# Performance work log

Hardware: AMD Instinct MI355X
Metric: run time of the kernel (lower is better)

## Reference

```python
import jax, jax.numpy as jnp
import numpy as np

B, D0, D1 = 4096, 128, 128
T, DEPTH, W = 64, 2, 4          # num_tree, depth, width
S = W ** (DEPTH + 1)            # num_state = 64
NODES = sum(W ** l for l in range(DEPTH + 1))  # 21 internal nodes per tree
D = D0 + D1


def setup_inputs() -> dict:
    key = jax.random.key(0)
    ks = jax.random.split(key, 9)
    inp0 = jax.random.normal(ks[0], (B, D0), jnp.float32)
    inp1 = jax.random.normal(ks[1], (B, D1), jnp.float32)
    x2 = jax.random.normal(ks[2], (B,), jnp.float32)
    # ForestLinear: per-tree, per-node linear maps to `width` branch logits
    W_nodes = 0.02 * jax.random.normal(ks[3], (T, NODES, D, W), jnp.float32)
    b_nodes = jnp.zeros((T, NODES, W), jnp.float32)
    # MultiDense([0,1], 1): per-(tree,state) linear probe per input
    W0 = 0.02 * jax.random.normal(ks[4], (T, S, D0), jnp.float32)
    b0 = jnp.zeros((T, S), jnp.float32)
    W1 = 0.02 * jax.random.normal(ks[5], (T, S, D1), jnp.float32)
    b1 = jnp.zeros((T, S), jnp.float32)
    return {"inp0": inp0, "inp1": inp1, "x2": x2,
            "W_nodes": W_nodes, "b_nodes": b_nodes,
            "W0": W0, "b0": b0, "W1": W1, "b1": b1}


def _forest_states(x, W_nodes, b_nodes):
    # x: [B, D] -> leaf-state probabilities [B, T, S]
    logits = jnp.einsum('bd,tndw->btnw', x, W_nodes) + b_nodes  # [B,T,NODES,W]
    probs = jax.nn.softmax(logits, axis=-1)
    p = jnp.ones((x.shape[0], T, 1), probs.dtype)
    off = 0
    for l in range(DEPTH + 1):
        n = W ** l
        pl = probs[:, :, off:off + n, :]                 # [B,T,n,W]
        p = (p[..., None] * pl).reshape(x.shape[0], T, n * W)
        off += n
    return p  # [B, T, S]


def reference(inp0, inp1, x2, W_nodes, b_nodes, W0, b0, W1, b1):
    x_states = _forest_states(jnp.concatenate([inp0, inp1], axis=-1), W_nodes, b_nodes)
    # per-tree/state linear probes; equivalent to tile + MultiDense, no materialized tile
    x_pred = (jnp.einsum('bd,tsd->bts', inp0, W0) + b0
              + jnp.einsum('bd,tsd->bts', inp1, W1) + b1)  # [B,T,S]
    y_pred_logit_parallel = x2[:, None, None] + x_pred
    ave_pred_tree = jnp.sum(x_states * jax.nn.sigmoid(y_pred_logit_parallel), axis=2)  # [B,T]
    ave_pred = jnp.mean(ave_pred_tree, axis=1)  # [B]
    return (y_pred_logit_parallel, ave_pred)
```

## Files before the change

kernel.cpp:

```cpp
#include <hip/hip_runtime.h>

#define B_SZ    4096
#define DD      256
#define T_TREES 64
#define NNODES  21
#define S_LEAF  64
#define NCOL_L  84
#define PRED_OFF 96
#define NCOL    160
#define M_TILE  128
#define HBYTES  (NCOL * 128 * 2)
#define WBYTES  (2 * HBYTES)
#define XOFF    ((size_t)T_TREES * WBYTES)
#define PRSTR   150

typedef __attribute__((ext_vector_type(8))) short  short8;
typedef __attribute__((ext_vector_type(4))) float  f32x4;

__device__ __forceinline__ unsigned short f2bf(float f) {
    unsigned int u = __float_as_uint(f);
    u += 0x7fffu + ((u >> 16) & 1u);
    return (unsigned short)(u >> 16);
}
__device__ __forceinline__ float bf2f(unsigned short u) {
    return __uint_as_float((unsigned int)u << 16);
}
__device__ __forceinline__ void gl2lds16(const void* g, void* l) {
    __builtin_amdgcn_global_load_lds(
        (const __attribute__((address_space(1))) unsigned int*)g,
        (__attribute__((address_space(3))) unsigned int*)l, 16, 0, 0);
}
__device__ __forceinline__ int woff(int c, int klo) {
    return c * 256 + ((klo ^ (c & 15)) << 4);
}

__global__ void zero_ave_kernel(float* __restrict__ out1) {
    int i = blockIdx.x * 256 + threadIdx.x;
    if (i < B_SZ) out1[i] = 0.0f;
}

__global__ void prep_weights(const float* __restrict__ Wn, const float* __restrict__ W0,
                             const float* __restrict__ W1, const float* __restrict__ inp0,
                             const float* __restrict__ inp1, char* __restrict__ ws,
                             float* __restrict__ out1) {
    int id = blockIdx.x * 256 + threadIdx.x;
    if (id < 43008) {
        int oct  = id & 31;
        int rest = id >> 5;
        int n    = rest % NNODES;
        int t    = rest / NNODES;
        int h    = oct >> 4, klo = oct & 15;
        const f32x4* src = (const f32x4*)(Wn + (((size_t)t * NNODES + n) * DD + oct * 8) * 4);
        f32x4 v[8];
        #pragma unroll
        for (int j = 0; j < 8; ++j) v[j] = src[j];
        char* base = ws + (size_t)t * WBYTES + h * HBYTES;
        #pragma unroll
        for (int w = 0; w < 4; ++w) {
            int c = n * 4 + w;
            short8 pack;
            #pragma unroll
            for (int j = 0; j < 8; ++j) pack[j] = (short)f2bf(v[j][w]);
            *(short8*)(base + woff(c, klo)) = pack;
        }
    } else if (id < 67584) {
        int idx  = id - 43008;
        int klo  = idx & 15;
        int h    = (idx >> 4) & 1;
        int rest = idx >> 5;
        int c    = NCOL_L + rest % 12;
        int t    = rest / 12;
        short8 z = (short8){0,0,0,0,0,0,0,0};
        *(short8*)(ws + (size_t)t * WBYTES + h * HBYTES + woff(c, klo)) = z;
    } else if (id < 198656) {
        int idx = id - 67584;
        int klo = idx & 15;
        int h   = (idx >> 4) & 1;
        int s   = (idx >> 5) & 63;
        int t   = idx >> 11;
        const float* src = (h == 0) ? (W0 + ((size_t)t * S_LEAF + s) * 128 + klo * 8)
                                    : (W1 + ((size_t)t * S_LEAF + s) * 128 + klo * 8);
        short8 pack;
        #pragma unroll
        for (int j = 0; j < 8; ++j) pack[j] = (short)f2bf(src[j]);
        *(short8*)(ws + (size_t)t * WBYTES + h * HBYTES + woff(PRED_OFF + s, klo)) = pack;
    } else if (id < 202752) {
        out1[id - 198656] = 0.0f;
    } else if (id < 333824) {
        int idx = id - 202752;
        int oct = idx & 31;
        int r   = idx >> 5;
        const float* src = (oct < 16) ? (inp0 + (size_t)r * 128 + oct * 8)
                                      : (inp1 + (size_t)r * 128 + (oct - 16) * 8);
        f32x4 f0 = *(const f32x4*)src;
        f32x4 f1 = *(const f32x4*)(src + 4);
        short8 pack;
        pack[0]=(short)f2bf(f0[0]); pack[1]=(short)f2bf(f0[1]);
        pack[2]=(short)f2bf(f0[2]); pack[3]=(short)f2bf(f0[3]);
        pack[4]=(short)f2bf(f1[0]); pack[5]=(short)f2bf(f1[1]);
        pack[6]=(short)f2bf(f1[2]); pack[7]=(short)f2bf(f1[3]);
        *(short8*)(ws + XOFF + ((size_t)r * DD + oct * 8) * 2) = pack;
    }
}

template<bool PRE>
__device__ __forceinline__ short8 ldA(const unsigned short* __restrict__ xbf,
                                      const float* __restrict__ inp0,
                                      const float* __restrict__ inp1,
                                      int gr, int kk, int kg) {
    if (PRE) {
        return *(const short8*)(xbf + (size_t)gr * DD + kk * 32 + kg * 8);
    } else {
        int k0 = kk * 32 + kg * 8;
        const float* src = (kk < 4) ? (inp0 + (size_t)gr * 128 + k0)
                                    : (inp1 + (size_t)gr * 128 + (k0 - 128));
        f32x4 f0 = *(const f32x4*)src;
        f32x4 f1 = *(const f32x4*)(src + 4);
        short8 a;
        a[0]=(short)f2bf(f0[0]); a[1]=(short)f2bf(f0[1]);
        a[2]=(short)f2bf(f0[2]); a[3]=(short)f2bf(f0[3]);
        a[4]=(short)f2bf(f1[0]); a[5]=(short)f2bf(f1[1]);
        a[6]=(short)f2bf(f1[2]); a[7]=(short)f2bf(f1[3]);
        return a;
    }
}

template<bool PRE>
__global__ __launch_bounds__(256, 4)
void forest_main(const float* __restrict__ inp0, const float* __restrict__ inp1,
                 const float* __restrict__ x2,   const float* __restrict__ Wn,
                 const float* __restrict__ bn,   const float* __restrict__ W0,
                 const float* __restrict__ b0,   const float* __restrict__ W1,
                 const float* __restrict__ b1,   const char* __restrict__ wsW,
                 float* __restrict__ out0, float* __restrict__ out1) {
    __shared__ __align__(16) char smem[HBYTES];

    const int tid  = threadIdx.x;
    const int orig = blockIdx.x;
    const int swz  = (orig & 7) * 256 + (orig >> 3);
    const int t    = swz >> 5;
    const int mt   = swz & 31;
    const int m0   = mt * M_TILE;
    const int lane = tid & 63;
    const int wid  = tid >> 6;
    const int ri   = lane & 15;
    const int kg   = lane >> 4;

    const unsigned short* xbf = (const unsigned short*)(wsW + XOFF);

    f32x4 acc[2][10];
    #pragma unroll
    for (int sr = 0; sr < 2; ++sr)
        #pragma unroll
        for (int ct = 0; ct < 10; ++ct)
            acc[sr][ct] = (f32x4){0.f, 0.f, 0.f, 0.f};

    const int baseRow = m0 + wid * 32;
    const int grA = baseRow + ri;
    const int grB = baseRow + 16 + ri;

    short8 aC0 = ldA<PRE>(xbf, inp0, inp1, grA, 0, kg);
    short8 aC1 = ldA<PRE>(xbf, inp0, inp1, grB, 0, kg);

    for (int h = 0; h < 2; ++h) {
        if (PRE) {
            const char* src = wsW + (size_t)t * WBYTES + h * HBYTES + tid * 16;
            char* dst = smem + tid * 16;
            #pragma unroll
            for (int it = 0; it < 10; ++it)
                gl2lds16(src + it * 4096, dst + it * 4096);
        } else {
            #pragma unroll
            for (int it = 0; it < 10; ++it) {
                int q   = tid + it * 256;
                int c   = q >> 4;
                int klo = q & 15;
                int k0  = h * 128 + klo * 8;
                unsigned short v[8];
                if (c < NCOL_L) {
                    int n = c >> 2, w = c & 3;
                    const float* src = Wn + (((size_t)t * NNODES + n) * DD + k0) * 4 + w;
                    #pragma unroll
                    for (int j = 0; j < 8; ++j) v[j] = f2bf(src[j * 4]);
                } else if (c < PRED_OFF) {
                    #pragma unroll
                    for (int j = 0; j < 8; ++j) v[j] = 0;
                } else {
                    int s = c - PRED_OFF;
                    const float* src = (k0 < 128) ? (W0 + ((size_t)t * S_LEAF + s) * 128 + k0)
                                                  : (W1 + ((size_t)t * S_LEAF + s) * 128 + (k0 - 128));
                    #pragma unroll
                    for (int j = 0; j < 8; ++j) v[j] = f2bf(src[j]);
                }
                short8 pack;
                #pragma unroll
                for (int j = 0; j < 8; ++j) pack[j] = (short)v[j];
                *(short8*)(smem + woff(c, klo)) = pack;
            }
        }
        __syncthreads();

        #pragma unroll
        for (int ks = 0; ks < 4; ++ks) {
            const int kk = h * 4 + ks;
            short8 aN0, aN1;
            if (kk < 7) {
                aN0 = ldA<PRE>(xbf, inp0, inp1, grA, kk + 1, kg);
                aN1 = ldA<PRE>(xbf, inp0, inp1, grB, kk + 1, kg);
            }
            #pragma unroll
            for (int ct = 0; ct < 10; ++ct) {
                short8 b = *(const short8*)(smem + woff(ct * 16 + ri, ks * 4 + kg));
                acc[0][ct] = __builtin_amdgcn_mfma_f32_16x16x32_bf16(aC0, b, acc[0][ct], 0, 0, 0);
                acc[1][ct] = __builtin_amdgcn_mfma_f32_16x16x32_bf16(aC1, b, acc[1][ct], 0, 0, 0);
            }
            aC0 = aN0; aC1 = aN1;
        }
        __syncthreads();
    }

    unsigned short* pr = (unsigned short*)smem;

    #pragma unroll
    for (int sr = 0; sr < 2; ++sr) {
        const int rlBase = wid * 32 + sr * 16 + kg * 4;
        #pragma unroll
        for (int ct = 0; ct < 6; ++ct) {
            int c = ct * 16 + ri;
            bool valid = (c < NCOL_L);
            float bnv = valid ? bn[t * NCOL_L + c] : 0.0f;
            #pragma unroll
            for (int r = 0; r < 4; ++r) {
                float v = acc[sr][ct][r] + bnv;
                float e = __expf(v);
                float ss = e + __shfl_xor(e, 1);
                ss += __shfl_xor(ss, 2);
                float p = e * __builtin_amdgcn_rcpf(ss);
                if (valid) pr[(rlBase + r) * PRSTR + c] = f2bf(p);
            }
        }
        const int gr0 = m0 + rlBase;
        float x2v0 = x2[gr0], x2v1 = x2[gr0 + 1], x2v2 = x2[gr0 + 2], x2v3 = x2[gr0 + 3];
        #pragma unroll
        for (int ct = 0; ct < 4; ++ct) {
            int s = ct * 16 + ri;
            float bb = b0[t * S_LEAF + s] + b1[t * S_LEAF + s];
            #pragma unroll
            for (int r = 0; r < 4; ++r) {
                float xv = (r == 0) ? x2v0 : (r == 1) ? x2v1 : (r == 2) ? x2v2 : x2v3;
                float y = acc[sr][ct + 6][r] + xv + bb;
                out0[((size_t)(gr0 + r) * T_TREES + t) * S_LEAF + s] = y;
                float sg = __builtin_amdgcn_rcpf(1.0f + __expf(-y));
                pr[(rlBase + r) * PRSTR + NCOL_L + s] = f2bf(sg);
            }
        }
    }
    __syncthreads();

    {
        int rl = wid * 32 + (lane >> 1);
        int hh = lane & 1;
        const unsigned short* prow = pr + (size_t)rl * PRSTR;
        float ssum = 0.0f;
        #pragma unroll
        for (int b8 = 0; b8 < 8; ++b8) {
            int b = hh * 8 + b8;
            float p01 = bf2f(prow[b >> 2]) * bf2f(prow[4 + b]);
            float inner = 0.0f;
            #pragma unroll
            for (int j = 0; j < 4; ++j) {
                int s = 4 * b + j;
                inner += bf2f(prow[20 + s]) * bf2f(prow[NCOL_L + s]);
            }
            ssum += p01 * inner;
        }
        ssum += __shfl_xor(ssum, 1);
        if (hh == 0) atomicAdd(out1 + (m0 + rl), ssum * (1.0f / T_TREES));
    }
}

extern "C" void kernel_launch(void* const* d_in, const int* in_sizes, int n_in,
                              void* d_out, int out_size, void* d_ws, size_t ws_size,
                              hipStream_t stream) {
    const float* inp0 = (const float*)d_in[0];
    const float* inp1 = (const float*)d_in[1];
    const float* x2   = (const float*)d_in[2];
    const float* Wn   = (const float*)d_in[3];
    const float* bn   = (const float*)d_in[4];
    const float* W0   = (const float*)d_in[5];
    const float* b0   = (const float*)d_in[6];
    const float* W1   = (const float*)d_in[7];
    const float* b1   = (const float*)d_in[8];

    float* out0 = (float*)d_out;
    float* out1 = out0 + (size_t)B_SZ * T_TREES * S_LEAF;

    const size_t need = XOFF + (size_t)B_SZ * DD * 2;
    dim3 grid((B_SZ / M_TILE) * T_TREES);

    if (ws_size >= need) {
        hipLaunchKernelGGL(prep_weights, dim3(1305), dim3(256), 0, stream,
                           Wn, W0, W1, inp0, inp1, (char*)d_ws, out1);
        hipLaunchKernelGGL((forest_main<true>), grid, dim3(256), 0, stream,
                           inp0, inp1, x2, Wn, bn, W0, b0, W1, b1,
                           (const char*)d_ws, out0, out1);
    } else {
        hipLaunchKernelGGL(zero_ave_kernel, dim3((B_SZ + 255) / 256), dim3(256), 0, stream, out1);
        hipLaunchKernelGGL((forest_main<false>), grid, dim3(256), 0, stream,
                           inp0, inp1, x2, Wn, bn, W0, b0, W1, b1,
                           (const char*)nullptr, out0, out1);
    }
}
```

Baseline: 55.74 us.

## Double-buffer K-quarter weight tiles and compute tree epilogue in registers via shuffles

Splits the per-tree weight slab into four K-quarters and double-buffers them in LDS, so the next quarter's global-to-LDS load overlaps the MFMAs of the current one. The column layout is reordered so level-0/1 nodes sit in the first tiles, with a new pair-interleaved swizzle. The epilogue no longer writes probabilities to LDS and rereads them after a barrier. It builds leaf path probabilities with cross-lane shuffles and reduces them into partial sums before the atomics. The cost is more barriers, more shuffle traffic and more register pressure.

```diff
diff --git a/kernel.cpp b/kernel.cpp
--- a/kernel.cpp
+++ b/kernel.cpp
@@ -5,14 +5,12 @@
 #define T_TREES 64
 #define NNODES  21
 #define S_LEAF  64
-#define NCOL_L  84
-#define PRED_OFF 96
 #define NCOL    160
 #define M_TILE  128
-#define HBYTES  (NCOL * 128 * 2)
-#define WBYTES  (2 * HBYTES)
+#define QBYTES  20480
+#define WBYTES  (4 * QBYTES)
 #define XOFF    ((size_t)T_TREES * WBYTES)
-#define PRSTR   150
+
 
 typedef __attribute__((ext_vector_type(8))) short  short8;
 typedef __attribute__((ext_vector_type(4))) float  f32x4;
@@ -22,16 +20,13 @@
     u += 0x7fffu + ((u >> 16) & 1u);
     return (unsigned short)(u >> 16);
 }
-__device__ __forceinline__ float bf2f(unsigned short u) {
-    return __uint_as_float((unsigned int)u << 16);
-}
 __device__ __forceinline__ void gl2lds16(const void* g, void* l) {
     __builtin_amdgcn_global_load_lds(
         (const __attribute__((address_space(1))) unsigned int*)g,
         (__attribute__((address_space(3))) unsigned int*)l, 16, 0, 0);
 }
-__device__ __forceinline__ int woff(int c, int klo) {
-    return c * 256 + ((klo ^ (c & 15)) << 4);
+__device__ __host__ __forceinline__ int woffq(int c, int klo) {
+    return (c >> 1) * 256 + (((((klo << 1) ^ (c & 14))) | (c & 1)) << 4);
 }
 
 __global__ void zero_ave_kernel(float* __restrict__ out1) {
@@ -49,41 +44,40 @@
         int rest = id >> 5;
         int n    = rest % NNODES;
         int t    = rest / NNODES;
-        int h    = oct >> 4, klo = oct & 15;
+        int q    = oct >> 3, klo = oct & 7;
         const f32x4* src = (const f32x4*)(Wn + (((size_t)t * NNODES + n) * DD + oct * 8) * 4);
         f32x4 v[8];
         #pragma unroll
         for (int j = 0; j < 8; ++j) v[j] = src[j];
-        char* base = ws + (size_t)t * WBYTES + h * HBYTES;
+        char* base = ws + (size_t)t * WBYTES + q * QBYTES;
         #pragma unroll
         for (int w = 0; w < 4; ++w) {
-            int c = n * 4 + w;
+            int c = n * 4 + w + (n >= 5 ? 12 : 0);
             short8 pack;
             #pragma unroll
             for (int j = 0; j < 8; ++j) pack[j] = (short)f2bf(v[j][w]);
-            *(short8*)(base + woff(c, klo)) = pack;
+            *(short8*)(base + woffq(c, klo)) = pack;
         }
     } else if (id < 67584) {
         int idx  = id - 43008;
-        int klo  = idx & 15;
-        int h    = (idx >> 4) & 1;
+        int kc   = idx & 31;
         int rest = idx >> 5;
-        int c    = NCOL_L + rest % 12;
+        int c    = 20 + rest % 12;
         int t    = rest / 12;
         short8 z = (short8){0,0,0,0,0,0,0,0};
-        *(short8*)(ws + (size_t)t * WBYTES + h * HBYTES + woff(c, klo)) = z;
+        *(short8*)(ws + (size_t)t * WBYTES + (kc >> 3) * QBYTES + woffq(c, kc & 7)) = z;
     } else if (id < 198656) {
         int idx = id - 67584;
-        int klo = idx & 15;
-        int h   = (idx >> 4) & 1;
+        int kc  = idx & 31;
         int s   = (idx >> 5) & 63;
         int t   = idx >> 11;
-        const float* src = (h == 0) ? (W0 + ((size_t)t * S_LEAF + s) * 128 + klo * 8)
-                                    : (W1 + ((size_t)t * S_LEAF + s) * 128 + klo * 8);
+        int k0  = kc * 8;
+        const float* src = (k0 < 128) ? (W0 + ((size_t)t * S_LEAF + s) * 128 + k0)
+                                      : (W1 + ((size_t)t * S_LEAF + s) * 128 + (k0 - 128));
         short8 pack;
         #pragma unroll
         for (int j = 0; j < 8; ++j) pack[j] = (short)f2bf(src[j]);
-        *(short8*)(ws + (size_t)t * WBYTES + h * HBYTES + woff(PRED_OFF + s, klo)) = pack;
+        *(short8*)(ws + (size_t)t * WBYTES + (kc >> 3) * QBYTES + woffq(96 + s, kc & 7)) = pack;
     } else if (id < 202752) {
         out1[id - 198656] = 0.0f;
     } else if (id < 333824) {
@@ -103,26 +97,20 @@
     }
 }
 
-template<bool PRE>
-__device__ __forceinline__ short8 ldA(const unsigned short* __restrict__ xbf,
-                                      const float* __restrict__ inp0,
-                                      const float* __restrict__ inp1,
-                                      int gr, int kk, int kg) {
-    if (PRE) {
-        return *(const short8*)(xbf + (size_t)gr * DD + kk * 32 + kg * 8);
-    } else {
-        int k0 = kk * 32 + kg * 8;
-        const float* src = (kk < 4) ? (inp0 + (size_t)gr * 128 + k0)
-                                    : (inp1 + (size_t)gr * 128 + (k0 - 128));
-        f32x4 f0 = *(const f32x4*)src;
-        f32x4 f1 = *(const f32x4*)(src + 4);
-        short8 a;
-        a[0]=(short)f2bf(f0[0]); a[1]=(short)f2bf(f0[1]);
-        a[2]=(short)f2bf(f0[2]); a[3]=(short)f2bf(f0[3]);
-        a[4]=(short)f2bf(f1[0]); a[5]=(short)f2bf(f1[1]);
-        a[6]=(short)f2bf(f1[2]); a[7]=(short)f2bf(f1[3]);
-        return a;
-    }
+__device__ __forceinline__ short8 ldAraw(const float* __restrict__ inp0,
+                                         const float* __restrict__ inp1,
+                                         int gr, int kkidx, int kg) {
+    int k0 = kkidx * 32 + kg * 8;
+    const float* src = (k0 < 128) ? (inp0 + (size_t)gr * 128 + k0)
+                                  : (inp1 + (size_t)gr * 128 + (k0 - 128));
+    f32x4 f0 = *(const f32x4*)src;
+    f32x4 f1 = *(const f32x4*)(src + 4);
+    short8 a;
+    a[0]=(short)f2bf(f0[0]); a[1]=(short)f2bf(f0[1]);
+    a[2]=(short)f2bf(f0[2]); a[3]=(short)f2bf(f0[3]);
+    a[4]=(short)f2bf(f1[0]); a[5]=(short)f2bf(f1[1]);
+    a[6]=(short)f2bf(f1[2]); a[7]=(short)f2bf(f1[3]);
+    return a;
 }
 
 template<bool PRE>
@@ -133,7 +121,7 @@
                  const float* __restrict__ b0,   const float* __restrict__ W1,
                  const float* __restrict__ b1,   const char* __restrict__ wsW,
                  float* __restrict__ out0, float* __restrict__ out1) {
-    __shared__ __align__(16) char smem[HBYTES];
+    __shared__ __align__(16) char smem[2 * QBYTES];
 
     const int tid  = threadIdx.x;
     const int orig = blockIdx.x;
@@ -155,38 +143,46 @@
         for (int ct = 0; ct < 10; ++ct)
             acc[sr][ct] = (f32x4){0.f, 0.f, 0.f, 0.f};
 
-    const int baseRow = m0 + wid * 32;
-    const int grA = baseRow + ri;
-    const int grB = baseRow + 16 + ri;
-
-    short8 aC0 = ldA<PRE>(xbf, inp0, inp1, grA, 0, kg);
-    short8 aC1 = ldA<PRE>(xbf, inp0, inp1, grB, 0, kg);
-
-    for (int h = 0; h < 2; ++h) {
+    const int gr0r = m0 + wid * 32 + ri;
+    const int gr1r = gr0r + 16;
+
+    int dsb[2];
+    #pragma unroll
+    for (int kkl = 0; kkl < 2; ++kkl) {
+        int klo = kkl * 4 + kg;
+        dsb[kkl] = (ri >> 1) * 256 + (((((klo << 1) ^ (ri & 14))) | (ri & 1)) << 4);
+    }
+
+    auto stageQ = [&](int q, int buf) {
         if (PRE) {
-            const char* src = wsW + (size_t)t * WBYTES + h * HBYTES + tid * 16;
-            char* dst = smem + tid * 16;
-            #pragma unroll
-            for (int it = 0; it < 10; ++it)
+            const char* src = wsW + (size_t)t * WBYTES + q * QBYTES + tid * 16;
+            char* dst = smem + buf * QBYTES + tid * 16;
+            #pragma unroll
+            for (int it = 0; it < 5; ++it)
                 gl2lds16(src + it * 4096, dst + it * 4096);
         } else {
             #pragma unroll
-            for (int it = 0; it < 10; ++it) {
-                int q   = tid + it * 256;
-                int c   = q >> 4;
-                int klo = q & 15;
-                int k0  = h * 128 + klo * 8;
+            for (int it = 0; it < 5; ++it) {
+                int idx = tid + it * 256;
+                int c   = idx >> 3;
+                int klo = idx & 7;
+                int k0  = (q * 8 + klo) * 8;
                 unsigned short v[8];
-                if (c < NCOL_L) {
+                if (c < 20) {
                     int n = c >> 2, w = c & 3;
                     const float* src = Wn + (((size_t)t * NNODES + n) * DD + k0) * 4 + w;
                     #pragma unroll
                     for (int j = 0; j < 8; ++j) v[j] = f2bf(src[j * 4]);
-                } else if (c < PRED_OFF) {
+                } else if (c < 32) {
                     #pragma unroll
                     for (int j = 0; j < 8; ++j) v[j] = 0;
+                } else if (c < 96) {
+                    int n = 5 + ((c - 32) >> 2), w = (c - 32) & 3;
+                    const float* src = Wn + (((size_t)t * NNODES + n) * DD + k0) * 4 + w;
+                    #pragma unroll
+                    for (int j = 0; j < 8; ++j) v[j] = f2bf(src[j * 4]);
                 } else {
-                    int s = c - PRED_OFF;
+                    int s = c - 96;
                     const float* src = (k0 < 128) ? (W0 + ((size_t)t * S_LEAF + s) * 128 + k0)
                                                   : (W1 + ((size_t)t * S_LEAF + s) * 128 + (k0 - 128));
                     #pragma unroll
@@ -195,87 +191,104 @@
                 short8 pack;
                 #pragma unroll
                 for (int j = 0; j < 8; ++j) pack[j] = (short)v[j];
-                *(short8*)(smem + woff(c, klo)) = pack;
+                *(short8*)(smem + buf * QBYTES + woffq(c, klo)) = pack;
             }
         }
+    };
+
+    stageQ(0, 0);
+    #pragma unroll
+    for (int q = 0; q < 4; ++q) {
         __syncthreads();
-
-        #pragma unroll
-        for (int ks = 0; ks < 4; ++ks) {
-            const int kk = h * 4 + ks;
-            short8 aN0, aN1;
-            if (kk < 7) {
-                aN0 = ldA<PRE>(xbf, inp0, inp1, grA, kk + 1, kg);
-                aN1 = ldA<PRE>(xbf, inp0, inp1, grB, kk + 1, kg);
-            }
-            #pragma unroll
-            for (int ct = 0; ct < 10; ++ct) {
-                short8 b = *(const short8*)(smem + woff(ct * 16 + ri, ks * 4 + kg));
-                acc[0][ct] = __builtin_amdgcn_mfma_f32_16x16x32_bf16(aC0, b, acc[0][ct], 0, 0, 0);
-                acc[1][ct] = __builtin_amdgcn_mfma_f32_16x16x32_bf16(aC1, b, acc[1][ct], 0, 0, 0);
-            }
-            aC0 = aN0; aC1 = aN1;
-        }
-        __syncthreads();
-    }
-
-    unsigned short* pr = (unsigned short*)smem;
-
+        short8 a00, a01, a10, a11;
+        if (PRE) {
+            a00 = *(const short8*)(xbf + (size_t)gr0r * DD + (2*q+0) * 32 + kg * 8);
+            a10 = *(const short8*)(xbf + (size_t)gr1r * DD + (2*q+0) * 32 + kg * 8);
+            a01 = *(const short8*)(xbf + (size_t)gr0r * DD + (2*q+1) * 32 + kg * 8);
+            a11 = *(const short8*)(xbf + (size_t)gr1r * DD + (2*q+1) * 32 + kg * 8);
+        } else {
+            a00 = ldAraw(inp0, inp1, gr0r, 2*q+0, kg);
+            a10 = ldAraw(inp0, inp1, gr1r, 2*q+0, kg);
+            a01 = ldAraw(inp0, inp1, gr0r, 2*q+1, kg);
+            a11 = ldAraw(inp0, inp1, gr1r, 2*q+1, kg);
+        }
+        if (q < 3) stageQ(q + 1, (q + 1) & 1);
+        const char* bufp = smem + (q & 1) * QBYTES;
+        #pragma unroll
+        for (int ct = 0; ct < 10; ++ct) {
+            short8 b0f = *(const short8*)(bufp + dsb[0] + ct * 2048);
+            acc[0][ct] = __builtin_amdgcn_mfma_f32_16x16x32_bf16(a00, b0f, acc[0][ct], 0, 0, 0);
+            acc[1][ct] = __builtin_amdgcn_mfma_f32_16x16x32_bf16(a10, b0f, acc[1][ct], 0, 0, 0);
+        }
+        #pragma unroll
+        for (int ct = 0; ct < 10; ++ct) {
+            short8 b1f = *(const short8*)(bufp + dsb[1] + ct * 2048);
+            acc[0][ct] = __builtin_amdgcn_mfma_f32_16x16x32_bf16(a01, b1f, acc[0][ct], 0, 0, 0);
+            acc[1][ct] = __builtin_amdgcn_mfma_f32_16x16x32_bf16(a11, b1f, acc[1][ct], 0, 0, 0);
+        }
+    }
+
+    const int kgbase = kg * 16;
     #pragma unroll
     for (int sr = 0; sr < 2; ++sr) {
         const int rlBase = wid * 32 + sr * 16 + kg * 4;
-        #pragma unroll
-        for (int ct = 0; ct < 6; ++ct) {
-            int c = ct * 16 + ri;
-            bool valid = (c < NCOL_L);
-            float bnv = valid ? bn[t * NCOL_L + c] : 0.0f;
+        const int gr0 = m0 + rlBase;
+        float x2v[4];
+        #pragma unroll
+        for (int r = 0; r < 4; ++r) x2v[r] = x2[gr0 + r];
+        float bn0 = bn[t * 84 + ri];
+        float bn1 = bn[t * 84 + 16 + (ri & 3)];
+
+        float L1r[4];
+        #pragma unroll
+        for (int r = 0; r < 4; ++r) {
+            float v0 = acc[sr][0][r] + bn0;
+            float e0 = __expf(v0);
+            float s0 = e0 + __shfl_xor(e0, 1); s0 += __shfl_xor(s0, 2);
+            float p0 = e0 * __builtin_amdgcn_rcpf(s0);
+            float v1 = acc[sr][1][r] + bn1;
+            float e1 = __expf(v1);
+            float s1 = e1 + __shfl_xor(e1, 1); s1 += __shfl_xor(s1, 2);
+            float p1 = e1 * __builtin_amdgcn_rcpf(s1);
+            float pa  = __shfl(p0, kgbase + (ri >> 2));
+            float pb0 = __shfl(p0, kgbase + ((ri + 4) & 15));
+            float pb1 = __shfl(p1, kgbase + ((ri + 4) & 15));
+            L1r[r] = pa * ((ri < 12) ? pb0 : pb1);
+        }
+        float L2v[4][4];
+        #pragma unroll
+        for (int ct2 = 0; ct2 < 4; ++ct2) {
+            float bn2 = bn[t * 84 + 20 + ct2 * 16 + ri];
             #pragma unroll
             for (int r = 0; r < 4; ++r) {
-                float v = acc[sr][ct][r] + bnv;
+                float v = acc[sr][2 + ct2][r] + bn2;
                 float e = __expf(v);
-                float ss = e + __shfl_xor(e, 1);
-                ss += __shfl_xor(ss, 2);
-                float p = e * __builtin_amdgcn_rcpf(ss);
-                if (valid) pr[(rlBase + r) * PRSTR + c] = f2bf(p);
+                float ss = e + __shfl_xor(e, 1); ss += __shfl_xor(ss, 2);
+                float p2 = e * __builtin_amdgcn_rcpf(ss);
+                float L1s = __shfl(L1r[r], kgbase + ct2 * 4 + (ri >> 2));
+                L2v[ct2][r] = p2 * L1s;
             }
         }
-        const int gr0 = m0 + rlBase;
-        float x2v0 = x2[gr0], x2v1 = x2[gr0 + 1], x2v2 = x2[gr0 + 2], x2v3 = x2[gr0 + 3];
+        float partial[4] = {0.f, 0.f, 0.f, 0.f};
         #pragma unroll
         for (int ct = 0; ct < 4; ++ct) {
             int s = ct * 16 + ri;
             float bb = b0[t * S_LEAF + s] + b1[t * S_LEAF + s];
             #pragma unroll
             for (int r = 0; r < 4; ++r) {
-                float xv = (r == 0) ? x2v0 : (r == 1) ? x2v1 : (r == 2) ? x2v2 : x2v3;
-                float y = acc[sr][ct + 6][r] + xv + bb;
+                float y = acc[sr][6 + ct][r] + x2v[r] + bb;
                 out0[((size_t)(gr0 + r) * T_TREES + t) * S_LEAF + s] = y;
                 float sg = __builtin_amdgcn_rcpf(1.0f + __expf(-y));
-                pr[(rlBase + r) * PRSTR + NCOL_L + s] = f2bf(sg);
+                partial[r] += sg * L2v[ct][r];
             }
         }
-    }
-    __syncthreads();
-
-    {
-        int rl = wid * 32 + (lane >> 1);
-        int hh = lane & 1;
-        const unsigned short* prow = pr + (size_t)rl * PRSTR;
-        float ssum = 0.0f;
-        #pragma unroll
-        for (int b8 = 0; b8 < 8; ++b8) {
-            int b = hh * 8 + b8;
-            float p01 = bf2f(prow[b >> 2]) * bf2f(prow[4 + b]);
-            float inner = 0.0f;
-            #pragma unroll
-            for (int j = 0; j < 4; ++j) {
-                int s = 4 * b + j;
-                inner += bf2f(prow[20 + s]) * bf2f(prow[NCOL_L + s]);
-            }
-            ssum += p01 * inner;
-        }
-        ssum += __shfl_xor(ssum, 1);
-        if (hh == 0) atomicAdd(out1 + (m0 + rl), ssum * (1.0f / T_TREES));
+        #pragma unroll
+        for (int r = 0; r < 4; ++r) {
+            float p = partial[r];
+            p += __shfl_xor(p, 1); p += __shfl_xor(p, 2);
+            p += __shfl_xor(p, 4); p += __shfl_xor(p, 8);
+            if (ri == 0) atomicAdd(out1 + gr0 + r, p * (1.0f / T_TREES));
+        }
     }
 }
 
@@ -299,7 +312,7 @@
     dim3 grid((B_SZ / M_TILE) * T_TREES);
 
     if (ws_size >= need) {
-        hipLaunchKernelGGL(prep_weights, dim3(1305), dim3(256), 0, stream,
+        hipLaunchKernelGGL(prep_weights, dim3(1304), dim3(256), 0, stream,
                            Wn, W0, W1, inp0, inp1, (char*)d_ws, out1);
         hipLaunchKernelGGL((forest_main<true>), grid, dim3(256), 0, stream,
                            inp0, inp1, x2, Wn, bn, W0, b0, W1, b1,
```

After: 69.81 us. +25.2%, slower.
